# Optimization experiments

Measured on AMD Instinct MI355X. Metric: run time of the kernel, lower is better.

The kernel has to match this reference:

```python
import jax, jax.numpy as jnp
import numpy as np

N, E, H, L, G = 50000, 500000, 128, 4, 1000
EPS = 1e-7      # GENConv message eps
LN_EPS = 1e-5   # torch LayerNorm default


def setup_inputs() -> dict:
    key = jax.random.key(0)
    ks = jax.random.split(key, 24)
    d = {}
    d["x"] = jax.random.normal(ks[0], (N, 9), jnp.float32)
    d["edge_index"] = jax.random.randint(ks[1], (2, E), 0, N, jnp.int32)
    d["edge_attr"] = jax.random.normal(ks[2], (E, 3), jnp.float32)
    d["batch"] = jnp.sort(jax.random.randint(ks[3], (N,), 0, G, jnp.int32))
    s9, s3, sh, s2h = 1/np.sqrt(9), 1/np.sqrt(3), 1/np.sqrt(H), 1/np.sqrt(2*H)
    u = lambda k, shp, s: jax.random.uniform(k, shp, jnp.float32, -s, s)
    d["enc_node_W"] = u(ks[4], (9, H), s9)
    d["enc_node_b"] = u(ks[5], (H,), s9)
    d["enc_edge_W"] = u(ks[6], (3, H), s3)
    d["enc_edge_b"] = u(ks[7], (H,), s3)
    d["ln_g"] = jnp.ones((L, H), jnp.float32)   # DeepGCNLayer pre-norm affine
    d["ln_b"] = jnp.zeros((L, H), jnp.float32)
    d["W1"] = u(ks[8], (L, H, 2*H), sh)          # GENConv MLP layer 1
    d["b1"] = u(ks[9], (L, 2*H), sh)
    d["mlp_ln_g"] = jnp.ones((L, 2*H), jnp.float32)
    d["mlp_ln_b"] = jnp.zeros((L, 2*H), jnp.float32)
    d["W2"] = u(ks[10], (L, 2*H, H), s2h)        # GENConv MLP layer 2
    d["b2"] = u(ks[11], (L, H), s2h)
    d["t"] = jnp.ones((L,), jnp.float32)         # learnable softmax temperature, init 1.0
    return d


def layernorm(x, g, b):
    mu = x.mean(-1, keepdims=True)
    var = ((x - mu) ** 2).mean(-1, keepdims=True)
    return (x - mu) / jnp.sqrt(var + LN_EPS) * g + b


def genconv(h, src, dst, ea, t, W1, b1, lg, lb, W2, b2):
    # message: relu(x_j + edge_attr) + eps   -> [E, H]
    msg = jax.nn.relu(h[src] + ea) + EPS
    # softmax aggregation over incoming edges, per channel
    logits = t * msg
    m = jax.ops.segment_max(logits, dst, num_segments=N)
    num = jnp.exp(logits - m[dst])
    den = jax.ops.segment_sum(num, dst, num_segments=N)
    alpha = num / den[dst]
    agg = jax.ops.segment_sum(msg * alpha, dst, num_segments=N)
    out = agg + h  # root residual inside GENConv
    z = jax.nn.relu(layernorm(out @ W1 + b1, lg, lb))
    return z @ W2 + b2


def reference(x, edge_index, edge_attr, batch, enc_node_W, enc_node_b,
              enc_edge_W, enc_edge_b, ln_g, ln_b, W1, b1, mlp_ln_g, mlp_ln_b,
              W2, b2, t):
    src, dst = edge_index[0], edge_index[1]
    h = x @ enc_node_W + enc_node_b            # node encoder  [N, H]
    ea = edge_attr @ enc_edge_W + enc_edge_b   # edge encoder  [E, H]
    # layer 0: conv only (DeeperGCN forward uses layers[0].conv directly)
    h = genconv(h, src, dst, ea, t[0], W1[0], b1[0], mlp_ln_g[0], mlp_ln_b[0], W2[0], b2[0])
    # layers 1..L-1: res+ block: x + conv(relu(LN(x))); dropout is identity (eval)
    for i in range(1, L):
        z = jax.nn.relu(layernorm(h, ln_g[i], ln_b[i]))
        h = h + genconv(z, src, dst, ea, t[i], W1[i], b1[i], mlp_ln_g[i], mlp_ln_b[i], W2[i], b2[i])
    h = jax.nn.relu(layernorm(h, ln_g[0], ln_b[0]))  # reuses layer-0 norm
    # global mean pool over graphs
    counts = jax.ops.segment_sum(jnp.ones((N,), h.dtype), batch, num_segments=G)
    sums = jax.ops.segment_sum(h, batch, num_segments=G)
    return sums / jnp.maximum(counts, 1.0)[:, None]
```

## Files before the change

kernel.cpp:

```cpp
#include <hip/hip_runtime.h>

#define NN 50000
#define NE 500000
#define HD 128
#define HD2 256
#define NL 4
#define NG 1000

constexpr float MSG_EPS = 1e-7f;
constexpr float LNEPS   = 1e-5f;

typedef float  f32x4  __attribute__((ext_vector_type(4)));
typedef __bf16 bf16x8 __attribute__((ext_vector_type(8)));

__device__ __forceinline__ unsigned short f2b(float f) {
    unsigned int u = __float_as_uint(f);
    unsigned int r = u + 0x7FFFu + ((u >> 16) & 1u);
    return (unsigned short)(r >> 16);
}
__device__ __forceinline__ float b2f(unsigned short h) {
    return __uint_as_float(((unsigned int)h) << 16);
}

__global__ void k_encode_nodes(const float* __restrict__ x, const float* __restrict__ W,
                               const float* __restrict__ b, unsigned short* __restrict__ zb) {
    int n = blockIdx.x;
    int c = threadIdx.x;
    float xr[9];
#pragma unroll
    for (int k = 0; k < 9; k++) xr[k] = x[n * 9 + k];
    float acc = b[c];
#pragma unroll
    for (int k = 0; k < 9; k++) acc = fmaf(xr[k], W[k * HD + c], acc);
    zb[n * HD + c] = f2b(acc);
}

__global__ void k_prep(const float* __restrict__ W1, const float* __restrict__ W2,
                       unsigned short* __restrict__ W1T, unsigned short* __restrict__ W2T) {
    int idx = blockIdx.x * 256 + threadIdx.x;
    {
        int k = idx & 127, n = (idx >> 7) & 255, l = idx >> 15;
        W1T[idx] = f2b(W1[(l * 128 + k) * 256 + n]);
    }
    {
        int k = idx & 255, n = (idx >> 8) & 127, l = idx >> 15;
        W2T[idx] = f2b(W2[(l * 256 + k) * 128 + n]);
    }
}

__global__ void k_hist(const int* __restrict__ dst, int* __restrict__ counts) {
    int e = blockIdx.x * blockDim.x + threadIdx.x;
    if (e < NE) atomicAdd(&counts[dst[e]], 1);
}

#define SCAN_B 512
__global__ void k_scan1(const int* __restrict__ counts, int* __restrict__ incl,
                        int* __restrict__ bsum) {
    __shared__ int s[SCAN_B];
    int i = blockIdx.x * SCAN_B + threadIdx.x;
    int v = (i < NN) ? counts[i] : 0;
    s[threadIdx.x] = v;
    __syncthreads();
    for (int off = 1; off < SCAN_B; off <<= 1) {
        int t = (threadIdx.x >= off) ? s[threadIdx.x - off] : 0;
        __syncthreads();
        s[threadIdx.x] += t;
        __syncthreads();
    }
    if (i < NN) incl[i] = s[threadIdx.x];
    if (threadIdx.x == SCAN_B - 1) bsum[blockIdx.x] = s[threadIdx.x];
}

__global__ void k_scan2(const int* __restrict__ bsum, int* __restrict__ boff, int nb) {
    __shared__ int s[128];
    int v = (threadIdx.x < nb) ? bsum[threadIdx.x] : 0;
    s[threadIdx.x] = v;
    __syncthreads();
    for (int off = 1; off < 128; off <<= 1) {
        int t = (threadIdx.x >= off) ? s[threadIdx.x - off] : 0;
        __syncthreads();
        s[threadIdx.x] += t;
        __syncthreads();
    }
    if (threadIdx.x < nb) boff[threadIdx.x] = s[threadIdx.x] - v;
}

__global__ void k_scan3(const int* __restrict__ incl, const int* __restrict__ boff,
                        int* __restrict__ row_start) {
    int i = blockIdx.x * SCAN_B + threadIdx.x;
    if (i < NN) row_start[i + 1] = incl[i] + boff[blockIdx.x];
    if (i == 0) row_start[0] = 0;
}

__global__ void k_scatter(const int* __restrict__ src, const int* __restrict__ dst,
                          const float* __restrict__ eattr, const int* __restrict__ row_start,
                          int* __restrict__ cursor, float4* __restrict__ aperm) {
    int e = blockIdx.x * blockDim.x + threadIdx.x;
    if (e >= NE) return;
    int d = dst[e];
    int p = row_start[d] + atomicAdd(&cursor[d], 1);
    float4 v;
    v.x = eattr[e * 3 + 0];
    v.y = eattr[e * 3 + 1];
    v.z = eattr[e * 3 + 2];
    v.w = __int_as_float(src[e]);
    aperm[p] = v;
}

__global__ __launch_bounds__(256) void k_aggregate(const unsigned short* __restrict__ zb,
                                                   const float4* __restrict__ aperm,
                                                   const int* __restrict__ row_start,
                                                   const float* __restrict__ We,
                                                   const float* __restrict__ be,
                                                   const float* __restrict__ t, int layer,
                                                   unsigned int* __restrict__ outb) {
    int w = threadIdx.x >> 6, lane = threadIdx.x & 63;
    int n = blockIdx.x * 4 + w;
    if (n >= NN) return;
    int c = lane * 2;
    float2 w0 = *(const float2*)&We[c];
    float2 w1 = *(const float2*)&We[HD + c];
    float2 w2 = *(const float2*)&We[2 * HD + c];
    float2 bb = *(const float2*)&be[c];
    float tv = t[layer];
    int s0 = row_start[n], s1 = row_start[n + 1];
    float num0 = 0.f, num1 = 0.f, wm0 = 0.f, wm1 = 0.f;
    const unsigned int* z32 = (const unsigned int*)zb;
    int p = s0;
    for (; p + 2 <= s1; p += 2) {
        float4 a0 = aperm[p];
        float4 a1 = aperm[p + 1];
        int sj0 = __float_as_int(a0.w);
        int sj1 = __float_as_int(a1.w);
        unsigned int za = z32[sj0 * 64 + lane];
        unsigned int zc = z32[sj1 * 64 + lane];
        float zax = b2f((unsigned short)za), zay = b2f((unsigned short)(za >> 16));
        float zcx = b2f((unsigned short)zc), zcy = b2f((unsigned short)(zc >> 16));
        float ea0x = fmaf(a0.x, w0.x, fmaf(a0.y, w1.x, fmaf(a0.z, w2.x, bb.x)));
        float ea0y = fmaf(a0.x, w0.y, fmaf(a0.y, w1.y, fmaf(a0.z, w2.y, bb.y)));
        float ea1x = fmaf(a1.x, w0.x, fmaf(a1.y, w1.x, fmaf(a1.z, w2.x, bb.x)));
        float ea1y = fmaf(a1.x, w0.y, fmaf(a1.y, w1.y, fmaf(a1.z, w2.y, bb.y)));
        float m0x = fmaxf(zax + ea0x, 0.f) + MSG_EPS;
        float m0y = fmaxf(zay + ea0y, 0.f) + MSG_EPS;
        float m1x = fmaxf(zcx + ea1x, 0.f) + MSG_EPS;
        float m1y = fmaxf(zcy + ea1y, 0.f) + MSG_EPS;
        float e0x = __expf(tv * m0x), e0y = __expf(tv * m0y);
        float e1x = __expf(tv * m1x), e1y = __expf(tv * m1y);
        num0 += e0x + e1x;
        num1 += e0y + e1y;
        wm0 = fmaf(m0x, e0x, fmaf(m1x, e1x, wm0));
        wm1 = fmaf(m0y, e0y, fmaf(m1y, e1y, wm1));
    }
    if (p < s1) {
        float4 a = aperm[p];
        int sj = __float_as_int(a.w);
        unsigned int za = z32[sj * 64 + lane];
        float zax = b2f((unsigned short)za), zay = b2f((unsigned short)(za >> 16));
        float eax = fmaf(a.x, w0.x, fmaf(a.y, w1.x, fmaf(a.z, w2.x, bb.x)));
        float eay = fmaf(a.x, w0.y, fmaf(a.y, w1.y, fmaf(a.z, w2.y, bb.y)));
        float mx = fmaxf(zax + eax, 0.f) + MSG_EPS;
        float my = fmaxf(zay + eay, 0.f) + MSG_EPS;
        float ex = __expf(tv * mx), ey = __expf(tv * my);
        num0 += ex;
        num1 += ey;
        wm0 = fmaf(mx, ex, wm0);
        wm1 = fmaf(my, ey, wm1);
    }
    unsigned int zn = z32[n * 64 + lane];
    float ox = ((s1 > s0) ? (wm0 / num0) : 0.f) + b2f((unsigned short)zn);
    float oy = ((s1 > s0) ? (wm1 / num1) : 0.f) + b2f((unsigned short)(zn >> 16));
    outb[n * 64 + lane] = (unsigned int)f2b(ox) | ((unsigned int)f2b(oy) << 16);
}

#define BM 32
#define HS_LD 264

__global__ __launch_bounds__(256) void k_mlp(const unsigned short* __restrict__ outb,
                                             const unsigned short* __restrict__ W1T,
                                             const float* __restrict__ b1l,
                                             const float* __restrict__ lgl,
                                             const float* __restrict__ lbl,
                                             const unsigned short* __restrict__ W2T,
                                             const float* __restrict__ b2l,
                                             float* __restrict__ h,
                                             const float* __restrict__ gn,
                                             const float* __restrict__ bn,
                                             unsigned short* __restrict__ zb,
                                             int add_residual) {
    __shared__ __align__(16) unsigned short Hs[BM * HS_LD];

    int nb = blockIdx.x * BM;
    int tid = threadIdx.x;
    int w = tid >> 6, lane = tid & 63, q = lane >> 4, i = lane & 15;

    f32x4 acc[2][4];
#pragma unroll
    for (int rt = 0; rt < 2; rt++)
#pragma unroll
        for (int ct = 0; ct < 4; ct++) acc[rt][ct] = (f32x4){0.f, 0.f, 0.f, 0.f};

#pragma unroll
    for (int ks = 0; ks < 4; ks++) {
        bf16x8 af[2], bf[4];
#pragma unroll
        for (int rt = 0; rt < 2; rt++) {
            int row = nb + rt * 16 + i;
            if (row < NN)
                af[rt] = *(const bf16x8*)&outb[(size_t)row * HD + ks * 32 + q * 8];
            else
                af[rt] = (bf16x8)(__bf16)0.f;
        }
#pragma unroll
        for (int ct = 0; ct < 4; ct++)
            bf[ct] = *(const bf16x8*)&W1T[(w * 64 + ct * 16 + i) * HD + ks * 32 + q * 8];
#pragma unroll
        for (int rt = 0; rt < 2; rt++)
#pragma unroll
            for (int ct = 0; ct < 4; ct++)
                acc[rt][ct] = __builtin_amdgcn_mfma_f32_16x16x32_bf16(af[rt], bf[ct],
                                                                     acc[rt][ct], 0, 0, 0);
    }

    float b1c[4];
#pragma unroll
    for (int ct = 0; ct < 4; ct++) b1c[ct] = b1l[w * 64 + ct * 16 + i];
#pragma unroll
    for (int rt = 0; rt < 2; rt++)
#pragma unroll
        for (int ct = 0; ct < 4; ct++)
#pragma unroll
            for (int r = 0; r < 4; r++)
                Hs[(rt * 16 + q * 4 + r) * HS_LD + w * 64 + ct * 16 + i] =
                    f2b(acc[rt][ct][r] + b1c[ct]);
    __syncthreads();

    {
        float4 g4 = *(const float4*)&lgl[lane * 4];
        float4 be4 = *(const float4*)&lbl[lane * 4];
        for (int r = 0; r < 8; r++) {
            int row = w * 8 + r;
            ushort4 hv = *(ushort4*)&Hs[row * HS_LD + lane * 4];
            float v0 = b2f(hv.x), v1 = b2f(hv.y), v2 = b2f(hv.z), v3 = b2f(hv.w);
            float s = v0 + v1 + v2 + v3;
            float sq = v0 * v0 + v1 * v1 + v2 * v2 + v3 * v3;
#pragma unroll
            for (int m = 32; m >= 1; m >>= 1) {
                s += __shfl_xor(s, m);
                sq += __shfl_xor(sq, m);
            }
            float mu = s * (1.f / 256.f);
            float var = sq * (1.f / 256.f) - mu * mu;
            float inv = rsqrtf(var + LNEPS);
            ushort4 o;
            o.x = f2b(fmaxf(fmaf((v0 - mu) * inv, g4.x, be4.x), 0.f));
            o.y = f2b(fmaxf(fmaf((v1 - mu) * inv, g4.y, be4.y), 0.f));
            o.z = f2b(fmaxf(fmaf((v2 - mu) * inv, g4.z, be4.z), 0.f));
            o.w = f2b(fmaxf(fmaf((v3 - mu) * inv, g4.w, be4.w), 0.f));
            *(ushort4*)&Hs[row * HS_LD + lane * 4] = o;
        }
    }
    __syncthreads();

    f32x4 acc2[2][2];
#pragma unroll
    for (int rt = 0; rt < 2; rt++)
#pragma unroll
        for (int ct = 0; ct < 2; ct++) acc2[rt][ct] = (f32x4){0.f, 0.f, 0.f, 0.f};

#pragma unroll
    for (int ks = 0; ks < 8; ks++) {
        bf16x8 af[2], bf[2];
#pragma unroll
        for (int rt = 0; rt < 2; rt++)
            af[rt] = *(const bf16x8*)&Hs[(rt * 16 + i) * HS_LD + ks * 32 + q * 8];
#pragma unroll
        for (int ct = 0; ct < 2; ct++)
            bf[ct] = *(const bf16x8*)&W2T[(w * 32 + ct * 16 + i) * HD2 + ks * 32 + q * 8];
#pragma unroll
        for (int rt = 0; rt < 2; rt++)
#pragma unroll
            for (int ct = 0; ct < 2; ct++)
                acc2[rt][ct] = __builtin_amdgcn_mfma_f32_16x16x32_bf16(af[rt], bf[ct],
                                                                      acc2[rt][ct], 0, 0, 0);
    }
    __syncthreads();

    float* Hsf = (float*)Hs;
    float b2c[2];
#pragma unroll
    for (int ct = 0; ct < 2; ct++) b2c[ct] = b2l[w * 32 + ct * 16 + i];
#pragma unroll
    for (int rt = 0; rt < 2; rt++)
#pragma unroll
        for (int ct = 0; ct < 2; ct++)
#pragma unroll
            for (int r = 0; r < 4; r++) {
                int rloc = rt * 16 + q * 4 + r;
                int row = nb + rloc;
                int col = w * 32 + ct * 16 + i;
                if (row < NN) {
                    size_t idx = (size_t)row * HD + col;
                    float v = acc2[rt][ct][r] + b2c[ct];
                    float hn = add_residual ? (h[idx] + v) : v;
                    h[idx] = hn;
                    Hsf[rloc * 132 + col] = hn;
                }
            }
    __syncthreads();

    {
        float2 gg = *(const float2*)&gn[lane * 2];
        float2 cc = *(const float2*)&bn[lane * 2];
        for (int rr = 0; rr < 8; rr++) {
            int rloc = w * 8 + rr;
            int row = nb + rloc;
            if (row >= NN) break;
            float2 v = *(float2*)&Hsf[rloc * 132 + lane * 2];
            float s = v.x + v.y, sq = v.x * v.x + v.y * v.y;
#pragma unroll
            for (int m = 32; m >= 1; m >>= 1) {
                s += __shfl_xor(s, m);
                sq += __shfl_xor(sq, m);
            }
            float mu = s * (1.f / 128.f);
            float var = sq * (1.f / 128.f) - mu * mu;
            float inv = rsqrtf(var + LNEPS);
            float z0 = fmaxf(fmaf((v.x - mu) * inv, gg.x, cc.x), 0.f);
            float z1 = fmaxf(fmaf((v.y - mu) * inv, gg.y, cc.y), 0.f);
            ((unsigned int*)zb)[(size_t)row * 64 + lane] =
                (unsigned int)f2b(z0) | ((unsigned int)f2b(z1) << 16);
        }
    }
}

__global__ void k_gbounds(const int* __restrict__ batch, int* __restrict__ gstart) {
    int g = blockIdx.x * blockDim.x + threadIdx.x;
    if (g > NG) return;
    int lo = 0, hi = NN;
    while (lo < hi) {
        int mid = (lo + hi) >> 1;
        if (batch[mid] < g) lo = mid + 1;
        else hi = mid;
    }
    gstart[g] = lo;
}

__global__ void k_pool(const unsigned short* __restrict__ zb, const int* __restrict__ gstart,
                       float* __restrict__ out) {
    int g = blockIdx.x;
    int c = threadIdx.x;
    int a = gstart[g], b = gstart[g + 1];
    float s0 = 0.f, s1 = 0.f;
    int n = a;
    for (; n + 2 <= b; n += 2) {
        s0 += b2f(zb[(size_t)n * HD + c]);
        s1 += b2f(zb[(size_t)(n + 1) * HD + c]);
    }
    if (n < b) s0 += b2f(zb[(size_t)n * HD + c]);
    out[g * HD + c] = (s0 + s1) / fmaxf((float)(b - a), 1.f);
}

extern "C" void kernel_launch(void* const* d_in, const int* in_sizes, int n_in, void* d_out,
                              int out_size, void* d_ws, size_t ws_size, hipStream_t stream) {
    const float* x     = (const float*)d_in[0];
    const int* ei      = (const int*)d_in[1];
    const float* eattr = (const float*)d_in[2];
    const int* batch   = (const int*)d_in[3];
    const float* encW  = (const float*)d_in[4];
    const float* encB  = (const float*)d_in[5];
    const float* eW    = (const float*)d_in[6];
    const float* eB    = (const float*)d_in[7];
    const float* ln_g  = (const float*)d_in[8];
    const float* ln_b  = (const float*)d_in[9];
    const float* W1    = (const float*)d_in[10];
    const float* b1    = (const float*)d_in[11];
    const float* mlg   = (const float*)d_in[12];
    const float* mlb   = (const float*)d_in[13];
    const float* W2    = (const float*)d_in[14];
    const float* b2    = (const float*)d_in[15];
    const float* t     = (const float*)d_in[16];
    const int* src = ei;
    const int* dst = ei + NE;

    char* w = (char*)d_ws;
    auto alloc = [&](size_t bytes) {
        char* p = w;
        w += (bytes + 255) & ~size_t(255);
        return p;
    };
    float* h             = (float*)alloc(sizeof(float) * NN * HD);
    unsigned short* zb   = (unsigned short*)alloc(sizeof(unsigned short) * NN * HD);
    unsigned int* outb   = (unsigned int*)alloc(sizeof(unsigned int) * NN * HD / 2);
    float4* aperm        = (float4*)alloc(sizeof(float4) * NE);
    int* row_start       = (int*)alloc(sizeof(int) * (NN + 1));
    int* counts          = (int*)alloc(sizeof(int) * NN);
    int* cursor          = (int*)alloc(sizeof(int) * NN);
    int* incl            = (int*)alloc(sizeof(int) * NN);
    int* bsum            = (int*)alloc(sizeof(int) * 128);
    int* boff            = (int*)alloc(sizeof(int) * 128);
    int* gstart          = (int*)alloc(sizeof(int) * (NG + 1));
    unsigned short* W1T  = (unsigned short*)alloc(sizeof(unsigned short) * NL * HD * HD2);
    unsigned short* W2T  = (unsigned short*)alloc(sizeof(unsigned short) * NL * HD2 * HD);

    hipMemsetAsync(counts, 0, sizeof(int) * NN, stream);
    hipMemsetAsync(cursor, 0, sizeof(int) * NN, stream);

    k_prep<<<512, 256, 0, stream>>>(W1, W2, W1T, W2T);
    k_encode_nodes<<<NN, HD, 0, stream>>>(x, encW, encB, zb);
    k_hist<<<(NE + 255) / 256, 256, 0, stream>>>(dst, counts);
    int nsb = (NN + SCAN_B - 1) / SCAN_B;
    k_scan1<<<nsb, SCAN_B, 0, stream>>>(counts, incl, bsum);
    k_scan2<<<1, 128, 0, stream>>>(bsum, boff, nsb);
    k_scan3<<<nsb, SCAN_B, 0, stream>>>(incl, boff, row_start);
    k_scatter<<<(NE + 255) / 256, 256, 0, stream>>>(src, dst, eattr, row_start, cursor, aperm);
    k_gbounds<<<(NG + 256) / 256, 256, 0, stream>>>(batch, gstart);

    for (int l = 0; l < NL; l++) {
        k_aggregate<<<(NN + 3) / 4, 256, 0, stream>>>(zb, aperm, row_start, eW, eB, t, l, outb);
        int ln_next = (l + 1) % NL;
        k_mlp<<<(NN + BM - 1) / BM, 256, 0, stream>>>(
            (const unsigned short*)outb, W1T + (size_t)l * HD * HD2, b1 + l * HD2,
            mlg + l * HD2, mlb + l * HD2, W2T + (size_t)l * HD2 * HD, b2 + l * HD, h,
            ln_g + ln_next * HD, ln_b + ln_next * HD, zb, l > 0);
    }
    k_pool<<<NG, HD, 0, stream>>>(zb, gstart, (float*)d_out);
}
```

Before: 558.8 us.

## Restructure MLP kernel to one wave per 16 rows with register LayerNorm

The MLP kernel is rewritten so each 64-thread block owns 16 rows and computes all 256 hidden columns in registers. Both LayerNorms are done directly on MFMA accumulators with 16-lane shuffles instead of round-tripping through shared memory, which removes most __syncthreads and LDS traffic. The residual stream h is now stored in bf16 instead of fp32 to halve its memory traffic, at the cost of accumulated rounding error across layers. Smaller blocks and higher register use per thread (16 accumulators) may lower occupancy, and W1/W2 are re-read by many more blocks.

```diff
diff --git a/kernel.cpp b/kernel.cpp
--- a/kernel.cpp
+++ b/kernel.cpp
@@ -172,163 +172,154 @@
     outb[n * 64 + lane] = (unsigned int)f2b(ox) | ((unsigned int)f2b(oy) << 16);
 }
 
-#define BM 32
-#define HS_LD 264
-
-__global__ __launch_bounds__(256) void k_mlp(const unsigned short* __restrict__ outb,
-                                             const unsigned short* __restrict__ W1T,
-                                             const float* __restrict__ b1l,
-                                             const float* __restrict__ lgl,
-                                             const float* __restrict__ lbl,
-                                             const unsigned short* __restrict__ W2T,
-                                             const float* __restrict__ b2l,
-                                             float* __restrict__ h,
-                                             const float* __restrict__ gn,
-                                             const float* __restrict__ bn,
-                                             unsigned short* __restrict__ zb,
-                                             int add_residual) {
-    __shared__ __align__(16) unsigned short Hs[BM * HS_LD];
-
-    int nb = blockIdx.x * BM;
-    int tid = threadIdx.x;
-    int w = tid >> 6, lane = tid & 63, q = lane >> 4, i = lane & 15;
-
-    f32x4 acc[2][4];
-#pragma unroll
-    for (int rt = 0; rt < 2; rt++)
-#pragma unroll
-        for (int ct = 0; ct < 4; ct++) acc[rt][ct] = (f32x4){0.f, 0.f, 0.f, 0.f};
+#define HS_LD 268
+
+__global__ __launch_bounds__(64) void k_mlp(const unsigned short* __restrict__ outb,
+                                            const unsigned short* __restrict__ W1T,
+                                            const float* __restrict__ b1l,
+                                            const float* __restrict__ lgl,
+                                            const float* __restrict__ lbl,
+                                            const unsigned short* __restrict__ W2T,
+                                            const float* __restrict__ b2l,
+                                            unsigned short* __restrict__ h,
+                                            const float* __restrict__ gn,
+                                            const float* __restrict__ bn,
+                                            unsigned short* __restrict__ zb,
+                                            int add_residual) {
+    __shared__ __align__(16) unsigned short Hs[16 * HS_LD];
+
+    int base = blockIdx.x * 16;
+    int lane = threadIdx.x;
+    int q = lane >> 4, i = lane & 15;
+
+    f32x4 acc[16];
+#pragma unroll
+    for (int ct = 0; ct < 16; ct++) acc[ct] = (f32x4){0.f, 0.f, 0.f, 0.f};
 
 #pragma unroll
     for (int ks = 0; ks < 4; ks++) {
-        bf16x8 af[2], bf[4];
-#pragma unroll
-        for (int rt = 0; rt < 2; rt++) {
-            int row = nb + rt * 16 + i;
-            if (row < NN)
-                af[rt] = *(const bf16x8*)&outb[(size_t)row * HD + ks * 32 + q * 8];
-            else
-                af[rt] = (bf16x8)(__bf16)0.f;
-        }
-#pragma unroll
-        for (int ct = 0; ct < 4; ct++)
-            bf[ct] = *(const bf16x8*)&W1T[(w * 64 + ct * 16 + i) * HD + ks * 32 + q * 8];
-#pragma unroll
-        for (int rt = 0; rt < 2; rt++)
-#pragma unroll
-            for (int ct = 0; ct < 4; ct++)
-                acc[rt][ct] = __builtin_amdgcn_mfma_f32_16x16x32_bf16(af[rt], bf[ct],
-                                                                     acc[rt][ct], 0, 0, 0);
-    }
-
-    float b1c[4];
-#pragma unroll
-    for (int ct = 0; ct < 4; ct++) b1c[ct] = b1l[w * 64 + ct * 16 + i];
-#pragma unroll
-    for (int rt = 0; rt < 2; rt++)
-#pragma unroll
-        for (int ct = 0; ct < 4; ct++)
-#pragma unroll
-            for (int r = 0; r < 4; r++)
-                Hs[(rt * 16 + q * 4 + r) * HS_LD + w * 64 + ct * 16 + i] =
-                    f2b(acc[rt][ct][r] + b1c[ct]);
-    __syncthreads();
+        bf16x8 a = *(const bf16x8*)&outb[(size_t)(base + i) * HD + ks * 32 + q * 8];
+#pragma unroll
+        for (int ct = 0; ct < 16; ct++) {
+            bf16x8 bfr = *(const bf16x8*)&W1T[(ct * 16 + i) * HD + ks * 32 + q * 8];
+            acc[ct] = __builtin_amdgcn_mfma_f32_16x16x32_bf16(a, bfr, acc[ct], 0, 0, 0);
+        }
+    }
+
+#pragma unroll
+    for (int ct = 0; ct < 16; ct++) {
+        float bb = b1l[ct * 16 + i];
+#pragma unroll
+        for (int r = 0; r < 4; r++) acc[ct][r] += bb;
+    }
 
     {
-        float4 g4 = *(const float4*)&lgl[lane * 4];
-        float4 be4 = *(const float4*)&lbl[lane * 4];
-        for (int r = 0; r < 8; r++) {
-            int row = w * 8 + r;
-            ushort4 hv = *(ushort4*)&Hs[row * HS_LD + lane * 4];
-            float v0 = b2f(hv.x), v1 = b2f(hv.y), v2 = b2f(hv.z), v3 = b2f(hv.w);
-            float s = v0 + v1 + v2 + v3;
-            float sq = v0 * v0 + v1 * v1 + v2 * v2 + v3 * v3;
-#pragma unroll
-            for (int m = 32; m >= 1; m >>= 1) {
-                s += __shfl_xor(s, m);
-                sq += __shfl_xor(sq, m);
-            }
-            float mu = s * (1.f / 256.f);
-            float var = sq * (1.f / 256.f) - mu * mu;
-            float inv = rsqrtf(var + LNEPS);
-            ushort4 o;
-            o.x = f2b(fmaxf(fmaf((v0 - mu) * inv, g4.x, be4.x), 0.f));
-            o.y = f2b(fmaxf(fmaf((v1 - mu) * inv, g4.y, be4.y), 0.f));
-            o.z = f2b(fmaxf(fmaf((v2 - mu) * inv, g4.z, be4.z), 0.f));
-            o.w = f2b(fmaxf(fmaf((v3 - mu) * inv, g4.w, be4.w), 0.f));
-            *(ushort4*)&Hs[row * HS_LD + lane * 4] = o;
-        }
-    }
-    __syncthreads();
-
-    f32x4 acc2[2][2];
-#pragma unroll
-    for (int rt = 0; rt < 2; rt++)
-#pragma unroll
-        for (int ct = 0; ct < 2; ct++) acc2[rt][ct] = (f32x4){0.f, 0.f, 0.f, 0.f};
+        float s[4] = {0.f, 0.f, 0.f, 0.f}, sq[4] = {0.f, 0.f, 0.f, 0.f};
+#pragma unroll
+        for (int ct = 0; ct < 16; ct++)
+#pragma unroll
+            for (int r = 0; r < 4; r++) {
+                s[r] += acc[ct][r];
+                sq[r] = fmaf(acc[ct][r], acc[ct][r], sq[r]);
+            }
+#pragma unroll
+        for (int m = 8; m >= 1; m >>= 1)
+#pragma unroll
+            for (int r = 0; r < 4; r++) {
+                s[r] += __shfl_xor(s[r], m);
+                sq[r] += __shfl_xor(sq[r], m);
+            }
+        float mu[4], inv[4];
+#pragma unroll
+        for (int r = 0; r < 4; r++) {
+            mu[r] = s[r] * (1.f / 256.f);
+            float var = sq[r] * (1.f / 256.f) - mu[r] * mu[r];
+            inv[r] = rsqrtf(var + LNEPS);
+        }
+#pragma unroll
+        for (int ct = 0; ct < 16; ct++) {
+            float g = lgl[ct * 16 + i];
+            float c = lbl[ct * 16 + i];
+#pragma unroll
+            for (int r = 0; r < 4; r++) {
+                float v = fmaxf(fmaf((acc[ct][r] - mu[r]) * inv[r], g, c), 0.f);
+                Hs[(q * 4 + r) * HS_LD + ct * 16 + i] = f2b(v);
+            }
+        }
+    }
+
+    f32x4 acc2[8];
+#pragma unroll
+    for (int ct = 0; ct < 8; ct++) acc2[ct] = (f32x4){0.f, 0.f, 0.f, 0.f};
 
 #pragma unroll
     for (int ks = 0; ks < 8; ks++) {
-        bf16x8 af[2], bf[2];
-#pragma unroll
-        for (int rt = 0; rt < 2; rt++)
-            af[rt] = *(const bf16x8*)&Hs[(rt * 16 + i) * HS_LD + ks * 32 + q * 8];
-#pragma unroll
-        for (int ct = 0; ct < 2; ct++)
-            bf[ct] = *(const bf16x8*)&W2T[(w * 32 + ct * 16 + i) * HD2 + ks * 32 + q * 8];
-#pragma unroll
-        for (int rt = 0; rt < 2; rt++)
-#pragma unroll
-            for (int ct = 0; ct < 2; ct++)
-                acc2[rt][ct] = __builtin_amdgcn_mfma_f32_16x16x32_bf16(af[rt], bf[ct],
-                                                                      acc2[rt][ct], 0, 0, 0);
-    }
-    __syncthreads();
-
-    float* Hsf = (float*)Hs;
-    float b2c[2];
-#pragma unroll
-    for (int ct = 0; ct < 2; ct++) b2c[ct] = b2l[w * 32 + ct * 16 + i];
-#pragma unroll
-    for (int rt = 0; rt < 2; rt++)
-#pragma unroll
-        for (int ct = 0; ct < 2; ct++)
-#pragma unroll
-            for (int r = 0; r < 4; r++) {
-                int rloc = rt * 16 + q * 4 + r;
-                int row = nb + rloc;
-                int col = w * 32 + ct * 16 + i;
-                if (row < NN) {
-                    size_t idx = (size_t)row * HD + col;
-                    float v = acc2[rt][ct][r] + b2c[ct];
-                    float hn = add_residual ? (h[idx] + v) : v;
-                    h[idx] = hn;
-                    Hsf[rloc * 132 + col] = hn;
-                }
-            }
-    __syncthreads();
+        bf16x8 a = *(const bf16x8*)&Hs[i * HS_LD + ks * 32 + q * 8];
+#pragma unroll
+        for (int ct = 0; ct < 8; ct++) {
+            bf16x8 bfr = *(const bf16x8*)&W2T[(ct * 16 + i) * HD2 + ks * 32 + q * 8];
+            acc2[ct] = __builtin_amdgcn_mfma_f32_16x16x32_bf16(a, bfr, acc2[ct], 0, 0, 0);
+        }
+    }
+
+    if (add_residual) {
+#pragma unroll
+        for (int ct = 0; ct < 8; ct++) {
+            float bb = b2l[ct * 16 + i];
+#pragma unroll
+            for (int r = 0; r < 4; r++) {
+                size_t idx = (size_t)(base + q * 4 + r) * HD + ct * 16 + i;
+                acc2[ct][r] += bb + b2f(h[idx]);
+            }
+        }
+    } else {
+#pragma unroll
+        for (int ct = 0; ct < 8; ct++) {
+            float bb = b2l[ct * 16 + i];
+#pragma unroll
+            for (int r = 0; r < 4; r++) acc2[ct][r] += bb;
+        }
+    }
+#pragma unroll
+    for (int ct = 0; ct < 8; ct++)
+#pragma unroll
+        for (int r = 0; r < 4; r++) {
+            size_t idx = (size_t)(base + q * 4 + r) * HD + ct * 16 + i;
+            h[idx] = f2b(acc2[ct][r]);
+        }
 
     {
-        float2 gg = *(const float2*)&gn[lane * 2];
-        float2 cc = *(const float2*)&bn[lane * 2];
-        for (int rr = 0; rr < 8; rr++) {
-            int rloc = w * 8 + rr;
-            int row = nb + rloc;
-            if (row >= NN) break;
-            float2 v = *(float2*)&Hsf[rloc * 132 + lane * 2];
-            float s = v.x + v.y, sq = v.x * v.x + v.y * v.y;
-#pragma unroll
-            for (int m = 32; m >= 1; m >>= 1) {
-                s += __shfl_xor(s, m);
-                sq += __shfl_xor(sq, m);
-            }
-            float mu = s * (1.f / 128.f);
-            float var = sq * (1.f / 128.f) - mu * mu;
-            float inv = rsqrtf(var + LNEPS);
-            float z0 = fmaxf(fmaf((v.x - mu) * inv, gg.x, cc.x), 0.f);
-            float z1 = fmaxf(fmaf((v.y - mu) * inv, gg.y, cc.y), 0.f);
-            ((unsigned int*)zb)[(size_t)row * 64 + lane] =
-                (unsigned int)f2b(z0) | ((unsigned int)f2b(z1) << 16);
+        float s[4] = {0.f, 0.f, 0.f, 0.f}, sq[4] = {0.f, 0.f, 0.f, 0.f};
+#pragma unroll
+        for (int ct = 0; ct < 8; ct++)
+#pragma unroll
+            for (int r = 0; r < 4; r++) {
+                s[r] += acc2[ct][r];
+                sq[r] = fmaf(acc2[ct][r], acc2[ct][r], sq[r]);
+            }
+#pragma unroll
+        for (int m = 8; m >= 1; m >>= 1)
+#pragma unroll
+            for (int r = 0; r < 4; r++) {
+                s[r] += __shfl_xor(s[r], m);
+                sq[r] += __shfl_xor(sq[r], m);
+            }
+        float mu[4], inv[4];
+#pragma unroll
+        for (int r = 0; r < 4; r++) {
+            mu[r] = s[r] * (1.f / 128.f);
+            float var = sq[r] * (1.f / 128.f) - mu[r] * mu[r];
+            inv[r] = rsqrtf(var + LNEPS);
+        }
+#pragma unroll
+        for (int ct = 0; ct < 8; ct++) {
+            float g = gn[ct * 16 + i];
+            float c = bn[ct * 16 + i];
+#pragma unroll
+            for (int r = 0; r < 4; r++) {
+                float v = fmaxf(fmaf((acc2[ct][r] - mu[r]) * inv[r], g, c), 0.f);
+                zb[(size_t)(base + q * 4 + r) * HD + ct * 16 + i] = f2b(v);
+            }
         }
     }
 }
@@ -388,7 +379,7 @@
         w += (bytes + 255) & ~size_t(255);
         return p;
     };
-    float* h             = (float*)alloc(sizeof(float) * NN * HD);
+    unsigned short* h    = (unsigned short*)alloc(sizeof(unsigned short) * NN * HD);
     unsigned short* zb   = (unsigned short*)alloc(sizeof(unsigned short) * NN * HD);
     unsigned int* outb   = (unsigned int*)alloc(sizeof(unsigned int) * NN * HD / 2);
     float4* aperm        = (float4*)alloc(sizeof(float4) * NE);
@@ -418,7 +409,7 @@
     for (int l = 0; l < NL; l++) {
         k_aggregate<<<(NN + 3) / 4, 256, 0, stream>>>(zb, aperm, row_start, eW, eB, t, l, outb);
         int ln_next = (l + 1) % NL;
-        k_mlp<<<(NN + BM - 1) / BM, 256, 0, stream>>>(
+        k_mlp<<<NN / 16, 64, 0, stream>>>(
             (const unsigned short*)outb, W1T + (size_t)l * HD * HD2, b1 + l * HD2,
             mlg + l * HD2, mlb + l * HD2, W2T + (size_t)l * HD2 * HD, b2 + l * HD, h,
             ln_g + ln_next * HD, ln_b + ln_next * HD, zb, l > 0);
```

Result: slower. 586.1 us (+4.9%).
